# Kernel optimization log

Measured on AMD Instinct MI355X. Metric: run time of the kernel, lower is better.

Reference implementation:

```python
import jax, jax.numpy as jnp
import numpy as np

B, Hs, Ws, DIM = 8, 32, 32, 768
NH, HD = 12, 64  # num_heads, head_dim


def get_rel_pos(size, rel_pos):
    # q_size == k_size == size; no interpolation branch needed
    coords = jnp.arange(size)[:, None] - jnp.arange(size)[None, :] + (size - 1)
    return rel_pos[coords]  # (size, size, head_dim)


def setup_inputs() -> dict:
    key = jax.random.key(0)
    ks = jax.random.split(key, 7)
    inv = 1.0 / np.sqrt(DIM)
    return {
        "x": jax.random.normal(ks[0], (B, Hs, Ws, DIM), jnp.float32),
        "qkv_w": jax.random.normal(ks[1], (3 * DIM, DIM), jnp.float32) * inv,
        "qkv_b": jax.random.normal(ks[2], (3 * DIM,), jnp.float32) * 0.02,
        "proj_w": jax.random.normal(ks[3], (DIM, DIM), jnp.float32) * inv,
        "proj_b": jax.random.normal(ks[4], (DIM,), jnp.float32) * 0.02,
        "rel_pos_h": jax.random.normal(ks[5], (2 * Hs - 1, HD), jnp.float32) * 0.02,
        "rel_pos_w": jax.random.normal(ks[6], (2 * Ws - 1, HD), jnp.float32) * 0.02,
    }


def reference(x, qkv_w, qkv_b, proj_w, proj_b, rel_pos_h, rel_pos_w):
    Bb, H, W, C = x.shape
    L = H * W
    scale = HD ** -0.5

    qkv = x @ qkv_w.T + qkv_b                       # (B,H,W,3C)
    qkv = qkv.reshape(Bb, L, 3, NH, HD).transpose(2, 0, 3, 1, 4)
    q, k, v = qkv[0], qkv[1], qkv[2]                # (B,NH,L,HD)

    # decomposed 2D relative position bias
    rel_h = get_rel_pos(H, rel_pos_h)               # (H,H,HD)
    rel_w = get_rel_pos(W, rel_pos_w)               # (W,W,HD)
    q5 = q.reshape(Bb, NH, H, W, HD)
    rel_h_attn = jnp.einsum('bnhwc,hkc->bnhwk', q5, rel_h)  # (B,NH,H,W,H)
    rel_w_attn = jnp.einsum('bnhwc,wkc->bnhwk', q5, rel_w)  # (B,NH,H,W,W)
    bias = rel_h_attn[..., :, None] + rel_w_attn[..., None, :]  # (B,NH,H,W,H,W)
    bias = bias.reshape(Bb, NH, L, L)

    scores = jnp.einsum('bnqd,bnkd->bnqk', q, k) * scale + bias
    attn = jax.nn.softmax(scores, axis=-1)
    out = jnp.einsum('bnqk,bnkd->bnqd', attn, v)    # (B,NH,L,HD)

    out = out.reshape(Bb, NH, H, W, HD).transpose(0, 2, 3, 1, 4).reshape(Bb, H, W, C)
    return out @ proj_w.T + proj_b
```

## Files before the change

kernel.cpp:

```cpp
#include <hip/hip_runtime.h>

typedef unsigned short u16;
typedef __bf16 bf16x8 __attribute__((ext_vector_type(8)));
typedef float f32x4 __attribute__((ext_vector_type(4)));

#define NHEAD 12
#define LQ 1024
#define HDIM 64
#define DIMM 768

__device__ __forceinline__ u16 f2b(float f) {
  unsigned u = __float_as_uint(f);
  u += 0x7fffu + ((u >> 16) & 1u);
  return (u16)(u >> 16);
}
__device__ __forceinline__ float b2f(u16 v) {
  return __uint_as_float(((unsigned)v) << 16);
}
__device__ __forceinline__ unsigned cvt_pk(float lo, float hi) {
  unsigned r;
  asm("v_cvt_pk_bf16_f32 %0, %1, %2" : "=v"(r) : "v"(lo), "v"(hi));
  return r;
}
__device__ __forceinline__ void async16(const void* g, void* l) {
  __builtin_amdgcn_global_load_lds(
      (const __attribute__((address_space(1))) void*)g,
      (__attribute__((address_space(3))) void*)l, 16, 0, 0);
}
__device__ __forceinline__ uint2 shfl_u2(uint2 v, int src) {
  uint2 r;
  r.x = (unsigned)__shfl((int)v.x, src, 64);
  r.y = (unsigned)__shfl((int)v.y, src, 64);
  return r;
}

__global__ __launch_bounds__(256) void cvt_kernel(const float* __restrict__ in,
                                                  u16* __restrict__ out, int n4) {
  int i = blockIdx.x * 256 + threadIdx.x;
  if (i >= n4) return;
  const float4 v = reinterpret_cast<const float4*>(in)[i];
  ushort4 o;
  o.x = f2b(v.x); o.y = f2b(v.y); o.z = f2b(v.z); o.w = f2b(v.w);
  reinterpret_cast<ushort4*>(out)[i] = o;
}

__global__ __launch_bounds__(256) void cvt_rel(const float* __restrict__ rph,
                                               const float* __restrict__ rpw,
                                               u16* __restrict__ rphb,
                                               u16* __restrict__ rpwb) {
  int i = blockIdx.x * 256 + threadIdx.x;
  int tab = i >> 12, idx = i & 4095;
  int m = idx >> 6, d = idx & 63;
  const float* src = tab ? rpw : rph;
  u16* dst = tab ? rpwb : rphb;
  dst[idx] = (m < 63) ? f2b(src[m * HDIM + d]) : (u16)0;
}

__global__ __launch_bounds__(256) void gemm_qkv(const u16* __restrict__ A,
                                                const u16* __restrict__ Bt,
                                                const float* __restrict__ bias,
                                                u16* __restrict__ qb,
                                                u16* __restrict__ kb,
                                                u16* __restrict__ vtb) {
  __shared__ u16 la[2][128 * 64];
  __shared__ u16 lb[2][128 * 64];
  const int K = DIMM;
  int t = threadIdx.x;
  int lane = t & 63, wv = t >> 6;
  int l15 = lane & 15, l4 = lane >> 4;
  int swz = (blockIdx.x & 7) * 144 + (blockIdx.x >> 3);
  int bm = swz / 18, bn = swz % 18;
  int m0 = bm * 128, n0 = bn * 128;
  int wm = (wv >> 1) * 64, wn = (wv & 1) * 64;

  auto stage = [&](int s, int buf) {
    int k0 = s * 64;
    #pragma unroll
    for (int i = 0; i < 4; ++i) {
      int c = i * 256 + t;
      int row = c >> 3, co = c & 7;
      int g = co ^ (row & 7);
      async16(A + (m0 + row) * K + k0 + g * 8, (char*)&la[buf][0] + c * 16);
      async16(Bt + (n0 + row) * K + k0 + g * 8, (char*)&lb[buf][0] + c * 16);
    }
  };

  f32x4 acc[4][4];
  #pragma unroll
  for (int i = 0; i < 4; ++i)
    #pragma unroll
    for (int j = 0; j < 4; ++j) acc[i][j] = {0.f, 0.f, 0.f, 0.f};

  stage(0, 0);
  #pragma unroll 2
  for (int s = 0; s < 12; ++s) {
    int cur = s & 1;
    __syncthreads();
    if (s + 1 < 12) stage(s + 1, cur ^ 1);
    bf16x8 af[4][2], bfr[4][2];
    #pragma unroll
    for (int mi = 0; mi < 4; ++mi) {
      int row = wm + mi * 16 + l15;
      #pragma unroll
      for (int ks2 = 0; ks2 < 2; ++ks2)
        af[mi][ks2] = *reinterpret_cast<const bf16x8*>(
            &la[cur][row * 64 + (((ks2 << 2) + l4) ^ (row & 7)) * 8]);
    }
    #pragma unroll
    for (int nj = 0; nj < 4; ++nj) {
      int row = wn + nj * 16 + l15;
      #pragma unroll
      for (int ks2 = 0; ks2 < 2; ++ks2)
        bfr[nj][ks2] = *reinterpret_cast<const bf16x8*>(
            &lb[cur][row * 64 + (((ks2 << 2) + l4) ^ (row & 7)) * 8]);
    }
    #pragma unroll
    for (int mi = 0; mi < 4; ++mi)
      #pragma unroll
      for (int nj = 0; nj < 4; ++nj)
        #pragma unroll
        for (int ks2 = 0; ks2 < 2; ++ks2)
          acc[mi][nj] = __builtin_amdgcn_mfma_f32_16x16x32_bf16(
              af[mi][ks2], bfr[nj][ks2], acc[mi][nj], 0, 0, 0);
  }

  int part = (n0 >> 7) / 6;
  #pragma unroll
  for (int nj = 0; nj < 4; ++nj) {
    int n = n0 + wn + nj * 16 + l15;
    float bv = bias[n];
    int d = n & 63;
    int head = (n >> 6) % NHEAD;
    #pragma unroll
    for (int mi = 0; mi < 4; ++mi) {
      #pragma unroll
      for (int r = 0; r < 4; ++r) {
        int m = m0 + wm + mi * 16 + l4 * 4 + r;
        int b = m >> 10, li = m & 1023;
        int bh = b * NHEAD + head;
        u16 o = f2b(acc[mi][nj][r] + bv);
        if (part == 0)      qb[(bh * LQ + li) * HDIM + d] = o;
        else if (part == 1) kb[(bh * LQ + li) * HDIM + d] = o;
        else                vtb[(bh * HDIM + d) * LQ + li] = o;
      }
    }
  }
}

__global__ __launch_bounds__(256) void attn_kernel(const u16* __restrict__ qb,
                                                   const u16* __restrict__ kb,
                                                   const u16* __restrict__ vtb,
                                                   const u16* __restrict__ rphb,
                                                   const u16* __restrict__ rpwb,
                                                   u16* __restrict__ ao) {
  __shared__ u16 lds_k[2][64 * 64];
  __shared__ u16 lds_v[2][64 * 64];
  __shared__ u16 lds_th[64 * 72];
  __shared__ u16 lds_tw[64 * 72];

  int swz = (blockIdx.x & 7) * 192 + (blockIdx.x >> 3);
  int bh = swz >> 4;
  int q0 = (swz & 15) * 64;
  int t = threadIdx.x;
  int wv = t >> 6, lane = t & 63;
  int l15 = lane & 15, l4 = lane >> 4;

  auto stagekv = [&](int kv0, int buf) {
    const u16* ks = kb + (bh * LQ + kv0) * HDIM;
    const u16* vs = vtb + bh * HDIM * LQ + kv0;
    #pragma unroll
    for (int i = 0; i < 2; ++i) {
      int c = i * 256 + t;
      int row = c >> 3, co = c & 7;
      int g = co ^ (row & 7);
      async16(ks + row * HDIM + g * 8, (char*)&lds_k[buf][0] + c * 16);
      async16(vs + row * LQ + g * 8, (char*)&lds_v[buf][0] + c * 16);
    }
  };

  stagekv(0, 0);

  bf16x8 qf[2];
  {
    const u16* qsrc = qb + (bh * LQ + q0 + wv * 16 + l15) * HDIM + l4 * 8;
    qf[0] = *reinterpret_cast<const bf16x8*>(qsrc);
    qf[1] = *reinterpret_cast<const bf16x8*>(qsrc + 32);
  }

  #pragma unroll
  for (int c = 0; c < 4; ++c) {
    f32x4 th = {0.f, 0.f, 0.f, 0.f}, tw = {0.f, 0.f, 0.f, 0.f};
    #pragma unroll
    for (int ks2 = 0; ks2 < 2; ++ks2) {
      bf16x8 bhf = *reinterpret_cast<const bf16x8*>(&rphb[(c * 16 + l15) * HDIM + ks2 * 32 + l4 * 8]);
      bf16x8 bwf = *reinterpret_cast<const bf16x8*>(&rpwb[(c * 16 + l15) * HDIM + ks2 * 32 + l4 * 8]);
      th = __builtin_amdgcn_mfma_f32_16x16x32_bf16(qf[ks2], bhf, th, 0, 0, 0);
      tw = __builtin_amdgcn_mfma_f32_16x16x32_bf16(qf[ks2], bwf, tw, 0, 0, 0);
    }
    #pragma unroll
    for (int r = 0; r < 4; ++r) {
      int row = wv * 16 + l4 * 4 + r;
      lds_th[row * 72 + c * 16 + l15] = f2b(th[r]);
      lds_tw[row * 72 + c * 16 + l15] = f2b(tw[r]);
    }
  }

  int gq = q0 + wv * 16 + l15;
  int hq = gq >> 5, wq = gq & 31;
  int lrow = wv * 16 + l15;
  const u16* thp = &lds_th[lrow * 72 + hq + 31];
  const u16* twp = &lds_tw[lrow * 72 + wq + 31];

  float tw_reg[8];
  #pragma unroll
  for (int j = 0; j < 8; ++j) {
    int k2 = (j >> 2) * 16 + l4 * 4 + (j & 3);
    tw_reg[j] = b2f(twp[-k2]);
  }

  float m_run = -1e30f, l_run = 0.f;
  f32x4 acc_o[4];
  #pragma unroll
  for (int dj = 0; dj < 4; ++dj) acc_o[dj] = {0.f, 0.f, 0.f, 0.f};

  int srcA = l15 + (l4 & 1) * 32;
  int srcB = srcA + 16;
  bool hiG = (l4 >> 1) & 1;

  #pragma unroll 2
  for (int cidx = 0; cidx < 16; ++cidx) {
    int cur = cidx & 1;
    int kv0 = cidx * 64;
    __syncthreads();
    if (cidx + 1 < 16) stagekv(kv0 + 64, cur ^ 1);

    f32x4 sc[4];
    __builtin_amdgcn_s_setprio(1);
    #pragma unroll
    for (int nj = 0; nj < 4; ++nj) {
      f32x4 a = {0.f, 0.f, 0.f, 0.f};
      #pragma unroll
      for (int ks2 = 0; ks2 < 2; ++ks2) {
        int co = (ks2 * 4 + l4) ^ (l15 & 7);
        bf16x8 kf = *reinterpret_cast<const bf16x8*>(&lds_k[cur][(nj * 16 + l15) * 64 + co * 8]);
        a = __builtin_amdgcn_mfma_f32_16x16x32_bf16(kf, qf[ks2], a, 0, 0, 0);
      }
      sc[nj] = a;
    }
    __builtin_amdgcn_s_setprio(0);

    int kv5 = kv0 >> 5;
    float th0 = b2f(thp[-kv5]);
    float th1 = b2f(thp[-kv5 - 1]);
    float p[4][4];
    float cmax = -1e30f;
    #pragma unroll
    for (int nj = 0; nj < 4; ++nj) {
      float thv = (nj < 2) ? th0 : th1;
      #pragma unroll
      for (int r = 0; r < 4; ++r) {
        float s = fmaf(sc[nj][r], 0.125f, thv) + tw_reg[(nj & 1) * 4 + r];
        p[nj][r] = s;
        cmax = fmaxf(cmax, s);
      }
    }
    cmax = fmaxf(cmax, __shfl_xor(cmax, 16));
    cmax = fmaxf(cmax, __shfl_xor(cmax, 32));

    if (!__all(cmax <= m_run + 8.0f)) {
      float mn = fmaxf(m_run, cmax);
      float scl = __expf(m_run - mn);
      m_run = mn;
      l_run *= scl;
      #pragma unroll
      for (int dj = 0; dj < 4; ++dj)
        #pragma unroll
        for (int r = 0; r < 4; ++r) acc_o[dj][r] *= scl;
    }

    float psum = 0.f;
    #pragma unroll
    for (int nj = 0; nj < 4; ++nj)
      #pragma unroll
      for (int r = 0; r < 4; ++r) {
        p[nj][r] = __expf(p[nj][r] - m_run);
        psum += p[nj][r];
      }
    psum += __shfl_xor(psum, 16);
    psum += __shfl_xor(psum, 32);
    l_run += psum;

    uint2 w4[4];
    #pragma unroll
    for (int nj = 0; nj < 4; ++nj) {
      w4[nj].x = cvt_pk(p[nj][0], p[nj][1]);
      w4[nj].y = cvt_pk(p[nj][2], p[nj][3]);
    }
    bf16x8 pf[2];
    #pragma unroll
    for (int ks2 = 0; ks2 < 2; ++ks2) {
      uint2 lo0 = shfl_u2(w4[ks2 * 2 + 0], srcA);
      uint2 lo1 = shfl_u2(w4[ks2 * 2 + 1], srcA);
      uint2 hi0 = shfl_u2(w4[ks2 * 2 + 0], srcB);
      uint2 hi1 = shfl_u2(w4[ks2 * 2 + 1], srcB);
      union { uint4 u; bf16x8 b; } cv;
      cv.u.x = hiG ? lo1.x : lo0.x;
      cv.u.y = hiG ? lo1.y : lo0.y;
      cv.u.z = hiG ? hi1.x : hi0.x;
      cv.u.w = hiG ? hi1.y : hi0.y;
      pf[ks2] = cv.b;
    }

    __builtin_amdgcn_s_setprio(1);
    #pragma unroll
    for (int dj = 0; dj < 4; ++dj) {
      int d = dj * 16 + l15;
      #pragma unroll
      for (int ks2 = 0; ks2 < 2; ++ks2) {
        int co = (ks2 * 4 + l4) ^ (l15 & 7);
        bf16x8 vf = *reinterpret_cast<const bf16x8*>(&lds_v[cur][d * 64 + co * 8]);
        acc_o[dj] = __builtin_amdgcn_mfma_f32_16x16x32_bf16(vf, pf[ks2], acc_o[dj], 0, 0, 0);
      }
    }
    __builtin_amdgcn_s_setprio(0);
  }

  int b = bh / NHEAD, head = bh % NHEAD;
  float inv = 1.f / l_run;
  u16* orow = ao + (b * LQ + gq) * DIMM + head * HDIM;
  #pragma unroll
  for (int dj = 0; dj < 4; ++dj) {
    uint2 pk;
    pk.x = cvt_pk(acc_o[dj][0] * inv, acc_o[dj][1] * inv);
    pk.y = cvt_pk(acc_o[dj][2] * inv, acc_o[dj][3] * inv);
    *reinterpret_cast<uint2*>(&orow[dj * 16 + l4 * 4]) = pk;
  }
}

__global__ __launch_bounds__(256) void gemm_proj(const u16* __restrict__ A,
                                                 const u16* __restrict__ Bt,
                                                 const float* __restrict__ bias,
                                                 float* __restrict__ out) {
  __shared__ u16 la[2][128 * 64];
  __shared__ u16 lb[2][128 * 64];
  const int K = DIMM;
  int t = threadIdx.x;
  int lane = t & 63, wv = t >> 6;
  int l15 = lane & 15, l4 = lane >> 4;
  int swz = (blockIdx.x & 7) * 48 + (blockIdx.x >> 3);
  int bm = swz / 6, bn = swz % 6;
  int m0 = bm * 128, n0 = bn * 128;
  int wm = (wv >> 1) * 64, wn = (wv & 1) * 64;

  auto stage = [&](int s, int buf) {
    int k0 = s * 64;
    #pragma unroll
    for (int i = 0; i < 4; ++i) {
      int c = i * 256 + t;
      int row = c >> 3, co = c & 7;
      int g = co ^ (row & 7);
      async16(A + (m0 + row) * K + k0 + g * 8, (char*)&la[buf][0] + c * 16);
      async16(Bt + (n0 + row) * K + k0 + g * 8, (char*)&lb[buf][0] + c * 16);
    }
  };

  f32x4 acc[4][4];
  #pragma unroll
  for (int i = 0; i < 4; ++i)
    #pragma unroll
    for (int j = 0; j < 4; ++j) acc[i][j] = {0.f, 0.f, 0.f, 0.f};

  stage(0, 0);
  #pragma unroll 2
  for (int s = 0; s < 12; ++s) {
    int cur = s & 1;
    __syncthreads();
    if (s + 1 < 12) stage(s + 1, cur ^ 1);
    bf16x8 af[4][2], bfr[4][2];
    #pragma unroll
    for (int mi = 0; mi < 4; ++mi) {
      int row = wm + mi * 16 + l15;
      #pragma unroll
      for (int ks2 = 0; ks2 < 2; ++ks2)
        af[mi][ks2] = *reinterpret_cast<const bf16x8*>(
            &la[cur][row * 64 + (((ks2 << 2) + l4) ^ (row & 7)) * 8]);
    }
    #pragma unroll
    for (int nj = 0; nj < 4; ++nj) {
      int row = wn + nj * 16 + l15;
      #pragma unroll
      for (int ks2 = 0; ks2 < 2; ++ks2)
        bfr[nj][ks2] = *reinterpret_cast<const bf16x8*>(
            &lb[cur][row * 64 + (((ks2 << 2) + l4) ^ (row & 7)) * 8]);
    }
    #pragma unroll
    for (int mi = 0; mi < 4; ++mi)
      #pragma unroll
      for (int nj = 0; nj < 4; ++nj)
        #pragma unroll
        for (int ks2 = 0; ks2 < 2; ++ks2)
          acc[mi][nj] = __builtin_amdgcn_mfma_f32_16x16x32_bf16(
              af[mi][ks2], bfr[nj][ks2], acc[mi][nj], 0, 0, 0);
  }

  #pragma unroll
  for (int nj = 0; nj < 4; ++nj) {
    int n = n0 + wn + nj * 16 + l15;
    float bv = bias[n];
    #pragma unroll
    for (int mi = 0; mi < 4; ++mi) {
      #pragma unroll
      for (int r = 0; r < 4; ++r) {
        int m = m0 + wm + mi * 16 + l4 * 4 + r;
        out[m * DIMM + n] = acc[mi][nj][r] + bv;
      }
    }
  }
}

extern "C" void kernel_launch(void* const* d_in, const int* in_sizes, int n_in,
                              void* d_out, int out_size, void* d_ws, size_t ws_size,
                              hipStream_t stream) {
  const float* x      = (const float*)d_in[0];
  const float* qkv_w  = (const float*)d_in[1];
  const float* qkv_b  = (const float*)d_in[2];
  const float* proj_w = (const float*)d_in[3];
  const float* proj_b = (const float*)d_in[4];
  const float* rph    = (const float*)d_in[5];
  const float* rpw    = (const float*)d_in[6];
  float* out = (float*)d_out;
  char* ws = (char*)d_ws;

  u16*   xb     = (u16*)(ws + 0);
  u16*   wqkvb  = (u16*)(ws + 12582912);
  u16*   wprojb = (u16*)(ws + 16121856);
  u16*   qb     = (u16*)(ws + 17301504);
  u16*   kb     = (u16*)(ws + 29884416);
  u16*   vtb    = (u16*)(ws + 42467328);
  u16*   rphb   = (u16*)(ws + 55050240);
  u16*   rpwb   = (u16*)(ws + 55058432);
  u16*   ao     = xb;

  cvt_kernel<<<6144, 256, 0, stream>>>(x, xb, 8192 * 768 / 4);
  cvt_kernel<<<1728, 256, 0, stream>>>(qkv_w, wqkvb, 2304 * 768 / 4);
  cvt_kernel<<<576, 256, 0, stream>>>(proj_w, wprojb, 768 * 768 / 4);
  cvt_rel<<<32, 256, 0, stream>>>(rph, rpw, rphb, rpwb);

  gemm_qkv<<<64 * 18, 256, 0, stream>>>(xb, wqkvb, qkv_b, qb, kb, vtb);

  attn_kernel<<<96 * 16, 256, 0, stream>>>(qb, kb, vtb, rphb, rpwb, ao);

  gemm_proj<<<64 * 6, 256, 0, stream>>>(ao, wprojb, proj_b, out);
}
```

Before: 164.9 us.

## Read K and V fragments directly from global memory instead of LDS staging

Removes the double-buffered async LDS staging of K and V tiles and the per-iteration block barrier. Each wave now loads its MFMA operand fragments for K and transposed V straight from global memory, relying on L1/L2 caching. This is meant to remove the barrier and LDS traffic, and to cut shared memory use so more blocks can be resident. In exchange, the four waves each fetch the same K/V data separately and nothing prefetches the next tile, so load latency is exposed.

```diff
diff --git a/kernel.cpp b/kernel.cpp
--- a/kernel.cpp
+++ b/kernel.cpp
@@ -153,8 +153,6 @@
                                                    const u16* __restrict__ rphb,
                                                    const u16* __restrict__ rpwb,
                                                    u16* __restrict__ ao) {
-  __shared__ u16 lds_k[2][64 * 64];
-  __shared__ u16 lds_v[2][64 * 64];
   __shared__ u16 lds_th[64 * 72];
   __shared__ u16 lds_tw[64 * 72];
 
@@ -165,21 +163,6 @@
   int wv = t >> 6, lane = t & 63;
   int l15 = lane & 15, l4 = lane >> 4;
 
-  auto stagekv = [&](int kv0, int buf) {
-    const u16* ks = kb + (bh * LQ + kv0) * HDIM;
-    const u16* vs = vtb + bh * HDIM * LQ + kv0;
-    #pragma unroll
-    for (int i = 0; i < 2; ++i) {
-      int c = i * 256 + t;
-      int row = c >> 3, co = c & 7;
-      int g = co ^ (row & 7);
-      async16(ks + row * HDIM + g * 8, (char*)&lds_k[buf][0] + c * 16);
-      async16(vs + row * LQ + g * 8, (char*)&lds_v[buf][0] + c * 16);
-    }
-  };
-
-  stagekv(0, 0);
-
   bf16x8 qf[2];
   {
     const u16* qsrc = qb + (bh * LQ + q0 + wv * 16 + l15) * HDIM + l4 * 8;
@@ -227,12 +210,11 @@
   int srcB = srcA + 16;
   bool hiG = (l4 >> 1) & 1;
 
-  #pragma unroll 2
+  const u16* kbase = kb + bh * LQ * HDIM;
+  const u16* vbase = vtb + bh * HDIM * LQ;
+
   for (int cidx = 0; cidx < 16; ++cidx) {
-    int cur = cidx & 1;
     int kv0 = cidx * 64;
-    __syncthreads();
-    if (cidx + 1 < 16) stagekv(kv0 + 64, cur ^ 1);
 
     f32x4 sc[4];
     __builtin_amdgcn_s_setprio(1);
@@ -241,8 +223,8 @@
       f32x4 a = {0.f, 0.f, 0.f, 0.f};
       #pragma unroll
       for (int ks2 = 0; ks2 < 2; ++ks2) {
-        int co = (ks2 * 4 + l4) ^ (l15 & 7);
-        bf16x8 kf = *reinterpret_cast<const bf16x8*>(&lds_k[cur][(nj * 16 + l15) * 64 + co * 8]);
+        bf16x8 kf = *reinterpret_cast<const bf16x8*>(
+            kbase + (kv0 + nj * 16 + l15) * HDIM + (ks2 * 4 + l4) * 8);
         a = __builtin_amdgcn_mfma_f32_16x16x32_bf16(kf, qf[ks2], a, 0, 0, 0);
       }
       sc[nj] = a;
@@ -314,11 +296,10 @@
     __builtin_amdgcn_s_setprio(1);
     #pragma unroll
     for (int dj = 0; dj < 4; ++dj) {
-      int d = dj * 16 + l15;
       #pragma unroll
       for (int ks2 = 0; ks2 < 2; ++ks2) {
-        int co = (ks2 * 4 + l4) ^ (l15 & 7);
-        bf16x8 vf = *reinterpret_cast<const bf16x8*>(&lds_v[cur][d * 64 + co * 8]);
+        bf16x8 vf = *reinterpret_cast<const bf16x8*>(
+            vbase + (dj * 16 + l15) * LQ + kv0 + (ks2 * 4 + l4) * 8);
         acc_o[dj] = __builtin_amdgcn_mfma_f32_16x16x32_bf16(vf, pf[ks2], acc_o[dj], 0, 0, 0);
       }
     }
```

Result: slower. 305.4 us (+85.2%).
